# Optimization experiments

Hardware: AMD Instinct MI355X
Metric: run time of the kernel (lower is better)

## Reference

```python
import jax, jax.numpy as jnp
import numpy as np

OUT_H, OUT_W = 7, 7
SCALE = 0.25
S = 2  # sample_num per bin axis


def _bilinear(img, y, x):
    """Bilinearly sample img[..., H, W] at float coords (y, x).
    y, x have identical shape G; returns img.shape[:-2] + G.
    Matches RoIAlign CUDA interpolation (zero outside [-1, H]/[-1, W])."""
    H, W = img.shape[-2], img.shape[-1]
    valid = (y > -1.0) & (y < H) & (x > -1.0) & (x < W)
    y = jnp.clip(y, 0.0, H - 1)
    x = jnp.clip(x, 0.0, W - 1)
    y0 = jnp.floor(y).astype(jnp.int32)
    x0 = jnp.floor(x).astype(jnp.int32)
    y1 = jnp.minimum(y0 + 1, H - 1)
    x1 = jnp.minimum(x0 + 1, W - 1)
    ly = y - y0
    lx = x - x0
    hy, hx = 1.0 - ly, 1.0 - lx
    v = (hy * hx * img[..., y0, x0] + hy * lx * img[..., y0, x1]
         + ly * hx * img[..., y1, x0] + ly * lx * img[..., y1, x1])
    return jnp.where(valid, v, 0.0)


def setup_inputs() -> dict:
    key = jax.random.key(0)
    k1, k2, k3, k4, k5 = jax.random.split(key, 5)
    N, C, H, W = 2, 256, 200, 200
    R, MH, MW = 512, 128, 128
    features = jax.random.normal(k1, (N, C, H, W), jnp.float32)
    bidx = jax.random.randint(k2, (R,), 0, N)
    xy1 = jax.random.randint(k3, (R, 2), 0, 672)          # x1, y1 (image coords)
    wh = jax.random.randint(k4, (R, 2), 8, 128)           # box sizes in [8,128)
    xy2 = jnp.minimum(xy1 + wh - 1, 799)                  # x2, y2 inclusive
    rois = jnp.concatenate([bidx[:, None].astype(jnp.float32),
                            xy1.astype(jnp.float32),
                            xy2.astype(jnp.float32)], axis=1)  # [R,5]
    batch_masks = jax.random.uniform(k5, (R, MH, MW), jnp.float32)
    # zero-pad beyond each roi's (h, w), mimicking the list->dense packing
    hv = jnp.arange(MH)[None, :] < (xy2[:, 1] - xy1[:, 1] + 1)[:, None]
    wv = jnp.arange(MW)[None, :] < (xy2[:, 0] - xy1[:, 0] + 1)[:, None]
    batch_masks = batch_masks * (hv[:, :, None] & wv[:, None, :]).astype(jnp.float32)
    return {"features": features, "rois": rois, "batch_masks": batch_masks}


def reference(features, rois, batch_masks):
    """Mask-weighted RoIAlign: per-roi bilinear feature samples are weighted by
    the roi's shape mask (bilinearly sampled in roi-relative image coords),
    then average-pooled over the sub-sample grid of each output bin."""
    C = features.shape[1]

    def one_roi(roi, mask):
        b = roi[0].astype(jnp.int32)
        x1, y1, x2, y2 = roi[1], roi[2], roi[3], roi[4]
        roi_start_w = x1 * SCALE
        roi_start_h = y1 * SCALE
        roi_w = jnp.maximum((x2 - x1 + 1.0) * SCALE, 1.0)
        roi_h = jnp.maximum((y2 - y1 + 1.0) * SCALE, 1.0)
        bin_w = roi_w / OUT_W
        bin_h = roi_h / OUT_H
        # sub-sample offsets: (bin + (i+0.5)/S) for i in [0,S)  -> [OUT*S]
        offs = (jnp.arange(S, dtype=jnp.float32) + 0.5) / S
        ys = roi_start_h + (jnp.arange(OUT_H, dtype=jnp.float32)[:, None] + offs[None, :]).reshape(-1) * bin_h
        xs = roi_start_w + (jnp.arange(OUT_W, dtype=jnp.float32)[:, None] + offs[None, :]).reshape(-1) * bin_w
        yy, xx = jnp.meshgrid(ys, xs, indexing='ij')       # [OUT_H*S, OUT_W*S]
        feat = features[b]                                  # [C, H, W]
        vals = _bilinear(feat, yy, xx)                      # [C, OUT_H*S, OUT_W*S]
        # mask weight at the same sample point, in roi-relative image coords
        my = jnp.clip(yy / SCALE - y1, 0.0, y2 - y1)
        mx = jnp.clip(xx / SCALE - x1, 0.0, x2 - x1)
        wgt = _bilinear(mask, my, mx)                       # [OUT_H*S, OUT_W*S]
        v = (vals * wgt).reshape(C, OUT_H, S, OUT_W, S)
        return v.mean(axis=(2, 4))                          # [C, OUT_H, OUT_W]

    return jax.vmap(one_roi)(rois, batch_masks)             # [R, C, OUT_H, OUT_W]
```

## Files before the change

### kernel.cpp

```cpp
#include <hip/hip_runtime.h>


constexpr int   OUT_H = 7, OUT_W = 7;
constexpr int   NBIN  = OUT_H * OUT_W;
constexpr float SCALE = 0.25f;
constexpr int   S     = 2;
constexpr int   NSAMP = NBIN * S * S;
constexpr int   CG    = 8;
constexpr int   RDIM  = 34;
constexpr int   RCOLS = 40;
constexpr int   CST   = RDIM * RCOLS + 4;

typedef unsigned short ushort_t;

__device__ __forceinline__ ushort_t f2bf(float f) {
    unsigned u = __float_as_uint(f);
    u += 0x7fffu + ((u >> 16) & 1u);
    return (ushort_t)(u >> 16);
}
__device__ __forceinline__ float bf2f(ushort_t h) {
    return __uint_as_float(((unsigned)h) << 16);
}

__global__ __launch_bounds__(256, 6)
void roialign_direct_kernel(const float* __restrict__ features,
                            const float* __restrict__ rois,
                            const float* __restrict__ masks,
                            float*       __restrict__ out,
                            int C, int H, int W, int MH, int MW) {
    __shared__ __align__(16) ushort_t s_reg[CG * CST];
    __shared__ ushort4 s_idx[NSAMP];
    __shared__ float4  s_w[NSAMP];

    const int r   = blockIdx.x;
    const int cg  = blockIdx.y;
    const int tid = threadIdx.x;

    const float* roi = rois + (size_t)r * 5;
    const int   b  = (int)roi[0];
    const float x1 = roi[1], y1 = roi[2], x2 = roi[3], y2 = roi[4];

    const float roi_start_w = x1 * SCALE;
    const float roi_start_h = y1 * SCALE;
    const float roi_w = fmaxf((x2 - x1 + 1.0f) * SCALE, 1.0f);
    const float roi_h = fmaxf((y2 - y1 + 1.0f) * SCALE, 1.0f);
    const float bin_w = roi_w * (1.0f / OUT_W);
    const float bin_h = roi_h * (1.0f / OUT_H);

    int y_lo = (int)floorf(roi_start_h); y_lo = max(0, min(y_lo, H - 1));
    int x_lo = (int)floorf(roi_start_w); x_lo = max(0, min(x_lo, W - 1));
    const int y_hi = max(y_lo, min((int)floorf(roi_start_h + roi_h) + 1, H - 1));
    const int x_hi = max(x_lo, min((int)floorf(roi_start_w + roi_w) + 1, W - 1));
    const int rows  = min(y_hi - y_lo + 1, RDIM);
    const int x_lo4 = x_lo & ~3;
    const int cols4 = min((x_hi - x_lo4 + 4) >> 2, RCOLS / 4);

    {
        const int c8   = tid >> 5;
        const int lane = tid & 31;
        const float* src = features + ((size_t)b * C + (size_t)(cg * CG + c8)) * (size_t)(H * W);
        ushort_t* dst = s_reg + c8 * CST;
        const int items = rows * cols4;
        for (int it = lane; it < items; it += 32) {
            const int ry = it / cols4;
            const int k  = it - ry * cols4;
            const float4 v = *(const float4*)(src + (size_t)(y_lo + ry) * W + x_lo4 + 4 * k);
            ushort4 h;
            h.x = f2bf(v.x); h.y = f2bf(v.y); h.z = f2bf(v.z); h.w = f2bf(v.w);
            *(ushort4*)(dst + ry * RCOLS + 4 * k) = h;
        }
    }

    if (tid < NSAMP) {
        const int bin = tid >> 2;
        const int sub = tid & 3;
        const int ph  = bin / OUT_W, pw = bin % OUT_W;
        const int iy  = sub >> 1,   ix = sub & 1;

        const float yy = roi_start_h + ((float)ph + ((float)iy + 0.5f) * (1.0f / S)) * bin_h;
        const float xx = roi_start_w + ((float)pw + ((float)ix + 0.5f) * (1.0f / S)) * bin_w;

        const bool valid = (yy > -1.0f) && (yy < (float)H) && (xx > -1.0f) && (xx < (float)W);

        const float* msk = masks + (size_t)r * MH * MW;
        float my = fminf(fmaxf(yy * (1.0f / SCALE) - y1, 0.0f), y2 - y1);
        float mx = fminf(fmaxf(xx * (1.0f / SCALE) - x1, 0.0f), x2 - x1);
        my = fminf(fmaxf(my, 0.0f), (float)(MH - 1));
        mx = fminf(fmaxf(mx, 0.0f), (float)(MW - 1));
        const int my0 = (int)floorf(my), mx0 = (int)floorf(mx);
        const int my1 = min(my0 + 1, MH - 1), mx1 = min(mx0 + 1, MW - 1);
        const float mly = my - (float)my0, mlx = mx - (float)mx0;
        const float mhy = 1.0f - mly,      mhx = 1.0f - mlx;
        const float wgt = mhy * mhx * msk[my0 * MW + mx0] + mhy * mlx * msk[my0 * MW + mx1]
                        + mly * mhx * msk[my1 * MW + mx0] + mly * mlx * msk[my1 * MW + mx1];

        const float yc = fminf(fmaxf(yy, 0.0f), (float)(H - 1));
        const float xc = fminf(fmaxf(xx, 0.0f), (float)(W - 1));
        const int y0  = (int)floorf(yc), x0 = (int)floorf(xc);
        const int y1i = min(y0 + 1, H - 1), x1i = min(x0 + 1, W - 1);
        const float ly = yc - (float)y0, lx = xc - (float)x0;
        const float hy = 1.0f - ly,      hx = 1.0f - lx;

        const int ly0 = min(max(y0  - y_lo,  0), RDIM  - 1);
        const int ly1 = min(max(y1i - y_lo,  0), RDIM  - 1);
        const int lx0 = min(max(x0  - x_lo4, 0), RCOLS - 1);
        const int lx1 = min(max(x1i - x_lo4, 0), RCOLS - 1);

        const float scale_all = (valid ? wgt : 0.0f) * (1.0f / (float)(S * S));
        ushort4 ix4;
        ix4.x = (ushort_t)(ly0 * RCOLS + lx0);
        ix4.y = (ushort_t)(ly0 * RCOLS + lx1);
        ix4.z = (ushort_t)(ly1 * RCOLS + lx0);
        ix4.w = (ushort_t)(ly1 * RCOLS + lx1);
        s_idx[tid] = ix4;
        float4 w4;
        w4.x = hy * hx * scale_all;
        w4.y = hy * lx * scale_all;
        w4.z = ly * hx * scale_all;
        w4.w = ly * lx * scale_all;
        s_w[tid] = w4;
    }
    __syncthreads();

    const int c  = tid & 7;
    const int sg = tid >> 3;
    const ushort_t* creg = s_reg + c * CST;

    float acc0 = 0.0f, acc1 = 0.0f;
#pragma unroll
    for (int sub = 0; sub < 4; ++sub) {
        const int s = sg * 4 + sub;
        const ushort4 ix = s_idx[s];
        const float4  w  = s_w[s];
        acc0 += w.x * bf2f(creg[ix.x]) + w.y * bf2f(creg[ix.y])
              + w.z * bf2f(creg[ix.z]) + w.w * bf2f(creg[ix.w]);
    }
    const int bin1 = sg + 32;
    if (bin1 < NBIN) {
#pragma unroll
        for (int sub = 0; sub < 4; ++sub) {
            const int s = bin1 * 4 + sub;
            const ushort4 ix = s_idx[s];
            const float4  w  = s_w[s];
            acc1 += w.x * bf2f(creg[ix.x]) + w.y * bf2f(creg[ix.y])
                  + w.z * bf2f(creg[ix.z]) + w.w * bf2f(creg[ix.w]);
        }
    }
    __syncthreads();

    float* s_out = (float*)s_reg;
    s_out[c * NBIN + sg] = acc0;
    if (bin1 < NBIN) s_out[c * NBIN + bin1] = acc1;
    __syncthreads();

    float* outr = out + ((size_t)r * C + (size_t)cg * CG) * NBIN;
    for (int i = tid; i < CG * NBIN; i += 256)
        outr[i] = s_out[i];
}

__global__ __launch_bounds__(256)
void mask_roialign_kernel(const float* __restrict__ features,
                          const float* __restrict__ rois,
                          const float* __restrict__ masks,
                          float*       __restrict__ out,
                          int C, int H, int W, int MH, int MW) {
    int blk = blockIdx.x;
    int pw  = blk % OUT_W;
    int ph  = (blk / OUT_W) % OUT_H;
    int r   = blk / (OUT_W * OUT_H);
    int c   = threadIdx.x;
    if (c >= C) return;

    const float* roi = rois + (size_t)r * 5;
    int   b  = (int)roi[0];
    float x1 = roi[1], y1 = roi[2], x2 = roi[3], y2 = roi[4];

    float roi_start_w = x1 * SCALE;
    float roi_start_h = y1 * SCALE;
    float roi_w = fmaxf((x2 - x1 + 1.0f) * SCALE, 1.0f);
    float roi_h = fmaxf((y2 - y1 + 1.0f) * SCALE, 1.0f);
    float bin_w = roi_w / (float)OUT_W;
    float bin_h = roi_h / (float)OUT_H;

    const float* fch = features + ((size_t)b * C + c) * (size_t)(H * W);
    const float* msk = masks + (size_t)r * MH * MW;

    float acc = 0.0f;
#pragma unroll
    for (int iy = 0; iy < S; ++iy) {
        float yy = roi_start_h + ((float)ph + ((float)iy + 0.5f) / (float)S) * bin_h;
#pragma unroll
        for (int ix = 0; ix < S; ++ix) {
            float xx = roi_start_w + ((float)pw + ((float)ix + 0.5f) / (float)S) * bin_w;
            bool valid = (yy > -1.0f) && (yy < (float)H) && (xx > -1.0f) && (xx < (float)W);
            float my = fminf(fmaxf(yy / SCALE - y1, 0.0f), fminf(y2 - y1, (float)(MH - 1)));
            float mx = fminf(fmaxf(xx / SCALE - x1, 0.0f), fminf(x2 - x1, (float)(MW - 1)));
            int my0 = (int)floorf(my), mx0 = (int)floorf(mx);
            int my1 = min(my0 + 1, MH - 1), mx1 = min(mx0 + 1, MW - 1);
            float mly = my - my0, mlx = mx - mx0, mhy = 1.0f - mly, mhx = 1.0f - mlx;
            float wgt = mhy * mhx * msk[my0 * MW + mx0] + mhy * mlx * msk[my0 * MW + mx1]
                      + mly * mhx * msk[my1 * MW + mx0] + mly * mlx * msk[my1 * MW + mx1];
            if (valid) {
                float yc = fminf(fmaxf(yy, 0.0f), (float)(H - 1));
                float xc = fminf(fmaxf(xx, 0.0f), (float)(W - 1));
                int y0 = (int)floorf(yc), x0 = (int)floorf(xc);
                int y1i = min(y0 + 1, H - 1), x1i = min(x0 + 1, W - 1);
                float ly = yc - y0, lx = xc - x0, hy = 1.0f - ly, hx = 1.0f - lx;
                float v = hy * hx * fch[y0  * W + x0 ] + hy * lx * fch[y0  * W + x1i]
                        + ly * hx * fch[y1i * W + x0 ] + ly * lx * fch[y1i * W + x1i];
                acc += wgt * v;
            }
        }
    }
    out[((size_t)r * C + c) * (size_t)NBIN + ph * OUT_W + pw] = acc * (1.0f / (S * S));
}

extern "C" void kernel_launch(void* const* d_in, const int* in_sizes, int n_in,
                              void* d_out, int out_size, void* d_ws, size_t ws_size,
                              hipStream_t stream) {
    const float* features = (const float*)d_in[0];
    const float* rois     = (const float*)d_in[1];
    const float* masks    = (const float*)d_in[2];
    float*       out      = (float*)d_out;

    const int R  = in_sizes[1] / 5;
    const int C  = out_size / (R * NBIN);
    const int H  = 200, W = 200;
    const int MH = 128, MW = 128;

    (void)d_ws; (void)ws_size;

    if ((C % CG == 0) && (W % 4 == 0)) {
        roialign_direct_kernel<<<dim3(R, C / CG), dim3(256), 0, stream>>>(
            features, rois, masks, out, C, H, W, MH, MW);
    } else {
        mask_roialign_kernel<<<dim3(R * NBIN), dim3(256), 0, stream>>>(
            features, rois, masks, out, C, H, W, MH, MW);
    }
}
```

Baseline: 186.6 us.

## Interleave channel pairs as packed bf16 in LDS and gather both per load

The shared-memory tile now stores two channels interleaved per pixel as a packed 32-bit bf16 pair. Each compute thread handles one channel pair and one bin, so every 32-bit LDS gather yields two channel values and halves the number of gathers. The staging loop loads the even and odd channel rows together and replaces the integer divide with a float-reciprocal estimate plus a correction step. The compute phase now uses only 196 of 256 threads, and the index offsets are prescaled to byte offsets.

```diff
diff --git a/kernel.cpp b/kernel.cpp
--- a/kernel.cpp
+++ b/kernel.cpp
@@ -7,9 +7,11 @@
 constexpr int   S     = 2;
 constexpr int   NSAMP = NBIN * S * S;
 constexpr int   CG    = 8;
+constexpr int   NPAIR = CG / 2;
 constexpr int   RDIM  = 34;
 constexpr int   RCOLS = 40;
-constexpr int   CST   = RDIM * RCOLS + 4;
+constexpr int   NPIX  = RDIM * RCOLS;
+constexpr int   PSTRIDE = NPIX * 2 + 4;
 
 typedef unsigned short ushort_t;
 
@@ -17,9 +19,6 @@
     unsigned u = __float_as_uint(f);
     u += 0x7fffu + ((u >> 16) & 1u);
     return (ushort_t)(u >> 16);
-}
-__device__ __forceinline__ float bf2f(ushort_t h) {
-    return __uint_as_float(((unsigned)h) << 16);
 }
 
 __global__ __launch_bounds__(256, 6)
@@ -28,7 +27,7 @@
                             const float* __restrict__ masks,
                             float*       __restrict__ out,
                             int C, int H, int W, int MH, int MW) {
-    __shared__ __align__(16) ushort_t s_reg[CG * CST];
+    __shared__ __align__(16) ushort_t s_reg[NPAIR * PSTRIDE];
     __shared__ ushort4 s_idx[NSAMP];
     __shared__ float4  s_w[NSAMP];
 
@@ -56,18 +55,32 @@
     const int cols4 = min((x_hi - x_lo4 + 4) >> 2, RCOLS / 4);
 
     {
-        const int c8   = tid >> 5;
+        const int g    = tid >> 5;
         const int lane = tid & 31;
-        const float* src = features + ((size_t)b * C + (size_t)(cg * CG + c8)) * (size_t)(H * W);
-        ushort_t* dst = s_reg + c8 * CST;
+        const int pr   = g >> 1;
+        const int part = g & 1;
+        const size_t HWs = (size_t)H * W;
+        const float* srcE = features + ((size_t)b * C + (size_t)(cg * CG + 2 * pr)) * HWs
+                          + (size_t)y_lo * W + x_lo4;
+        const float* srcO = srcE + HWs;
+        unsigned* dp32base = (unsigned*)(s_reg + pr * PSTRIDE);
         const int items = rows * cols4;
-        for (int it = lane; it < items; it += 32) {
-            const int ry = it / cols4;
-            const int k  = it - ry * cols4;
-            const float4 v = *(const float4*)(src + (size_t)(y_lo + ry) * W + x_lo4 + 4 * k);
-            ushort4 h;
-            h.x = f2bf(v.x); h.y = f2bf(v.y); h.z = f2bf(v.z); h.w = f2bf(v.w);
-            *(ushort4*)(dst + ry * RCOLS + 4 * k) = h;
+        const float rcp = 1.0f / (float)cols4;
+        for (int it = lane + part * 32; it < items; it += 64) {
+            int ry = (int)((float)it * rcp);
+            int k  = it - ry * cols4;
+            if (k >= cols4) { ry++; k -= cols4; }
+            if (k < 0)      { ry--; k += cols4; }
+            const float4 vE = *(const float4*)(srcE + ry * W + 4 * k);
+            const float4 vO = *(const float4*)(srcO + ry * W + 4 * k);
+            const int pix = ry * RCOLS + 4 * k;
+            uint2 a, c2;
+            a.x  = (unsigned)f2bf(vE.x) | ((unsigned)f2bf(vO.x) << 16);
+            a.y  = (unsigned)f2bf(vE.y) | ((unsigned)f2bf(vO.y) << 16);
+            c2.x = (unsigned)f2bf(vE.z) | ((unsigned)f2bf(vO.z) << 16);
+            c2.y = (unsigned)f2bf(vE.w) | ((unsigned)f2bf(vO.w) << 16);
+            *(uint2*)(dp32base + pix)     = a;
+            *(uint2*)(dp32base + pix + 2) = c2;
         }
     }
 
@@ -108,10 +121,10 @@
 
         const float scale_all = (valid ? wgt : 0.0f) * (1.0f / (float)(S * S));
         ushort4 ix4;
-        ix4.x = (ushort_t)(ly0 * RCOLS + lx0);
-        ix4.y = (ushort_t)(ly0 * RCOLS + lx1);
-        ix4.z = (ushort_t)(ly1 * RCOLS + lx0);
-        ix4.w = (ushort_t)(ly1 * RCOLS + lx1);
+        ix4.x = (ushort_t)((ly0 * RCOLS + lx0) * 4);
+        ix4.y = (ushort_t)((ly0 * RCOLS + lx1) * 4);
+        ix4.z = (ushort_t)((ly1 * RCOLS + lx0) * 4);
+        ix4.w = (ushort_t)((ly1 * RCOLS + lx1) * 4);
         s_idx[tid] = ix4;
         float4 w4;
         w4.x = hy * hx * scale_all;
@@ -122,35 +135,37 @@
     }
     __syncthreads();
 
-    const int c  = tid & 7;
-    const int sg = tid >> 3;
-    const ushort_t* creg = s_reg + c * CST;
-
-    float acc0 = 0.0f, acc1 = 0.0f;
-#pragma unroll
-    for (int sub = 0; sub < 4; ++sub) {
-        const int s = sg * 4 + sub;
-        const ushort4 ix = s_idx[s];
-        const float4  w  = s_w[s];
-        acc0 += w.x * bf2f(creg[ix.x]) + w.y * bf2f(creg[ix.y])
-              + w.z * bf2f(creg[ix.z]) + w.w * bf2f(creg[ix.w]);
-    }
-    const int bin1 = sg + 32;
-    if (bin1 < NBIN) {
+    float accE = 0.0f, accO = 0.0f;
+    const int pr  = tid & 3;
+    const int bin = tid >> 2;
+    if (tid < NSAMP) {
+        const char* base = (const char*)s_reg + pr * (PSTRIDE * 2);
 #pragma unroll
         for (int sub = 0; sub < 4; ++sub) {
-            const int s = bin1 * 4 + sub;
-            const ushort4 ix = s_idx[s];
-            const float4  w  = s_w[s];
-            acc1 += w.x * bf2f(creg[ix.x]) + w.y * bf2f(creg[ix.y])
-                  + w.z * bf2f(creg[ix.z]) + w.w * bf2f(creg[ix.w]);
+            const int s = bin * 4 + sub;
+            const ushort4 off = s_idx[s];
+            const float4  w   = s_w[s];
+            const unsigned q0 = *(const unsigned*)(base + off.x);
+            const unsigned q1 = *(const unsigned*)(base + off.y);
+            const unsigned q2 = *(const unsigned*)(base + off.z);
+            const unsigned q3 = *(const unsigned*)(base + off.w);
+            accE = fmaf(w.x, __uint_as_float(q0 << 16),          accE);
+            accO = fmaf(w.x, __uint_as_float(q0 & 0xffff0000u),  accO);
+            accE = fmaf(w.y, __uint_as_float(q1 << 16),          accE);
+            accO = fmaf(w.y, __uint_as_float(q1 & 0xffff0000u),  accO);
+            accE = fmaf(w.z, __uint_as_float(q2 << 16),          accE);
+            accO = fmaf(w.z, __uint_as_float(q2 & 0xffff0000u),  accO);
+            accE = fmaf(w.w, __uint_as_float(q3 << 16),          accE);
+            accO = fmaf(w.w, __uint_as_float(q3 & 0xffff0000u),  accO);
         }
     }
     __syncthreads();
 
     float* s_out = (float*)s_reg;
-    s_out[c * NBIN + sg] = acc0;
-    if (bin1 < NBIN) s_out[c * NBIN + bin1] = acc1;
+    if (tid < NSAMP) {
+        s_out[(2 * pr + 0) * NBIN + bin] = accE;
+        s_out[(2 * pr + 1) * NBIN + bin] = accO;
+    }
     __syncthreads();
 
     float* outr = out + ((size_t)r * C + (size_t)cg * CG) * NBIN;
```

New measurement: 179.1 us. 4.0% less time.

## Stage fp32 feature tiles via direct global-to-LDS loads and reorder grid

Applied to the files above, without the earlier changes.

Replaces the register-staged bf16 conversion of the feature tile with asynchronous global_load_lds transfers that write fp32 rows straight into shared memory, using a compact per-roi row stride. Mask loads are issued before the feature copy so their latency overlaps it, and sample offsets are now byte offsets into the fp32 tile. The grid is transposed so the channel-group blocks of the same roi are adjacent, which may improve locality, and the occupancy hint is lowered to fit the doubled LDS footprint. This removes the bf16 rounding and its conversion cost, but it doubles shared memory per block and reduces how many blocks can be resident.

```diff
diff --git a/kernel.cpp b/kernel.cpp
--- a/kernel.cpp
+++ b/kernel.cpp
@@ -8,32 +8,24 @@
 constexpr int   NSAMP = NBIN * S * S;
 constexpr int   CG    = 8;
 constexpr int   RDIM  = 34;
-constexpr int   RCOLS = 40;
-constexpr int   CST   = RDIM * RCOLS + 4;
+constexpr int   RCOLS4 = 10;
+constexpr int   MAXIT  = RDIM * RCOLS4;
+constexpr int   CH_DW  = MAXIT * 4 + 4;
 
 typedef unsigned short ushort_t;
 
-__device__ __forceinline__ ushort_t f2bf(float f) {
-    unsigned u = __float_as_uint(f);
-    u += 0x7fffu + ((u >> 16) & 1u);
-    return (ushort_t)(u >> 16);
-}
-__device__ __forceinline__ float bf2f(ushort_t h) {
-    return __uint_as_float(((unsigned)h) << 16);
-}
-
-__global__ __launch_bounds__(256, 6)
+__global__ __launch_bounds__(256, 3)
 void roialign_direct_kernel(const float* __restrict__ features,
                             const float* __restrict__ rois,
                             const float* __restrict__ masks,
                             float*       __restrict__ out,
                             int C, int H, int W, int MH, int MW) {
-    __shared__ __align__(16) ushort_t s_reg[CG * CST];
+    __shared__ __align__(16) float s_reg[CG * CH_DW];
     __shared__ ushort4 s_idx[NSAMP];
     __shared__ float4  s_w[NSAMP];
 
-    const int r   = blockIdx.x;
-    const int cg  = blockIdx.y;
+    const int cgp = blockIdx.x;
+    const int r   = blockIdx.y;
     const int tid = threadIdx.x;
 
     const float* roi = rois + (size_t)r * 5;
@@ -53,34 +45,18 @@
     const int x_hi = max(x_lo, min((int)floorf(roi_start_w + roi_w) + 1, W - 1));
     const int rows  = min(y_hi - y_lo + 1, RDIM);
     const int x_lo4 = x_lo & ~3;
-    const int cols4 = min((x_hi - x_lo4 + 4) >> 2, RCOLS / 4);
-
-    {
-        const int c8   = tid >> 5;
-        const int lane = tid & 31;
-        const float* src = features + ((size_t)b * C + (size_t)(cg * CG + c8)) * (size_t)(H * W);
-        ushort_t* dst = s_reg + c8 * CST;
-        const int items = rows * cols4;
-        for (int it = lane; it < items; it += 32) {
-            const int ry = it / cols4;
-            const int k  = it - ry * cols4;
-            const float4 v = *(const float4*)(src + (size_t)(y_lo + ry) * W + x_lo4 + 4 * k);
-            ushort4 h;
-            h.x = f2bf(v.x); h.y = f2bf(v.y); h.z = f2bf(v.z); h.w = f2bf(v.w);
-            *(ushort4*)(dst + ry * RCOLS + 4 * k) = h;
-        }
-    }
-
+    const int cols4 = min((x_hi - x_lo4 + 4) >> 2, RCOLS4);
+    const int rs_dw = cols4 << 2;
+
+    float yy = 0.f, xx = 0.f, m00 = 0.f, m01 = 0.f, m10 = 0.f, m11 = 0.f;
+    float mly = 0.f, mlx = 0.f;
     if (tid < NSAMP) {
         const int bin = tid >> 2;
         const int sub = tid & 3;
         const int ph  = bin / OUT_W, pw = bin % OUT_W;
         const int iy  = sub >> 1,   ix = sub & 1;
-
-        const float yy = roi_start_h + ((float)ph + ((float)iy + 0.5f) * (1.0f / S)) * bin_h;
-        const float xx = roi_start_w + ((float)pw + ((float)ix + 0.5f) * (1.0f / S)) * bin_w;
-
-        const bool valid = (yy > -1.0f) && (yy < (float)H) && (xx > -1.0f) && (xx < (float)W);
+        yy = roi_start_h + ((float)ph + ((float)iy + 0.5f) * (1.0f / S)) * bin_h;
+        xx = roi_start_w + ((float)pw + ((float)ix + 0.5f) * (1.0f / S)) * bin_w;
 
         const float* msk = masks + (size_t)r * MH * MW;
         float my = fminf(fmaxf(yy * (1.0f / SCALE) - y1, 0.0f), y2 - y1);
@@ -89,10 +65,49 @@
         mx = fminf(fmaxf(mx, 0.0f), (float)(MW - 1));
         const int my0 = (int)floorf(my), mx0 = (int)floorf(mx);
         const int my1 = min(my0 + 1, MH - 1), mx1 = min(mx0 + 1, MW - 1);
-        const float mly = my - (float)my0, mlx = mx - (float)mx0;
-        const float mhy = 1.0f - mly,      mhx = 1.0f - mlx;
-        const float wgt = mhy * mhx * msk[my0 * MW + mx0] + mhy * mlx * msk[my0 * MW + mx1]
-                        + mly * mhx * msk[my1 * MW + mx0] + mly * mlx * msk[my1 * MW + mx1];
+        mly = my - (float)my0; mlx = mx - (float)mx0;
+        m00 = msk[my0 * MW + mx0];
+        m01 = msk[my0 * MW + mx1];
+        m10 = msk[my1 * MW + mx0];
+        m11 = msk[my1 * MW + mx1];
+    }
+
+    {
+        const int wv   = tid >> 6;
+        const int lane = tid & 63;
+        const int items = rows * cols4;
+        const int nch   = (items + 63) >> 6;
+        const int imax  = max(items - 64, 0);
+        const float rcp = 1.0f / (float)cols4;
+        const size_t HWs = (size_t)H * W;
+#pragma unroll
+        for (int cc = 0; cc < 2; ++cc) {
+            const int ch = 2 * wv + cc;
+            const float* src0 = features
+                + ((size_t)b * C + (size_t)(cgp * CG + ch)) * HWs
+                + (size_t)y_lo * W + x_lo4;
+            float* lbase = s_reg + ch * CH_DW;
+            for (int j = 0; j < nch; ++j) {
+                const int bi = min(j << 6, imax);
+                const int it = min(bi + lane, items - 1);
+                int ry = (int)((float)it * rcp);
+                int k  = it - ry * cols4;
+                if (k < 0)           { --ry; k += cols4; }
+                else if (k >= cols4) { ++ry; k -= cols4; }
+                const float* src = src0 + (ry * W + (k << 2));
+                __builtin_amdgcn_global_load_lds(
+                    (const __attribute__((address_space(1))) unsigned int*)src,
+                    (__attribute__((address_space(3))) unsigned int*)(lbase + (bi << 2)),
+                    16, 0, 0);
+            }
+        }
+    }
+
+    if (tid < NSAMP) {
+        const bool valid = (yy > -1.0f) && (yy < (float)H) && (xx > -1.0f) && (xx < (float)W);
+        const float mhy = 1.0f - mly, mhx = 1.0f - mlx;
+        const float wgt = mhy * mhx * m00 + mhy * mlx * m01
+                        + mly * mhx * m10 + mly * mlx * m11;
 
         const float yc = fminf(fmaxf(yy, 0.0f), (float)(H - 1));
         const float xc = fminf(fmaxf(xx, 0.0f), (float)(W - 1));
@@ -101,18 +116,18 @@
         const float ly = yc - (float)y0, lx = xc - (float)x0;
         const float hy = 1.0f - ly,      hx = 1.0f - lx;
 
-        const int ly0 = min(max(y0  - y_lo,  0), RDIM  - 1);
-        const int ly1 = min(max(y1i - y_lo,  0), RDIM  - 1);
-        const int lx0 = min(max(x0  - x_lo4, 0), RCOLS - 1);
-        const int lx1 = min(max(x1i - x_lo4, 0), RCOLS - 1);
+        const int ly0 = min(max(y0  - y_lo,  0), rows - 1);
+        const int ly1 = min(max(y1i - y_lo,  0), rows - 1);
+        const int lx0 = min(max(x0  - x_lo4, 0), rs_dw - 1);
+        const int lx1 = min(max(x1i - x_lo4, 0), rs_dw - 1);
 
         const float scale_all = (valid ? wgt : 0.0f) * (1.0f / (float)(S * S));
-        ushort4 ix4;
-        ix4.x = (ushort_t)(ly0 * RCOLS + lx0);
-        ix4.y = (ushort_t)(ly0 * RCOLS + lx1);
-        ix4.z = (ushort_t)(ly1 * RCOLS + lx0);
-        ix4.w = (ushort_t)(ly1 * RCOLS + lx1);
-        s_idx[tid] = ix4;
+        ushort4 o;
+        o.x = (ushort_t)((ly0 * rs_dw + lx0) << 2);
+        o.y = (ushort_t)((ly0 * rs_dw + lx1) << 2);
+        o.z = (ushort_t)((ly1 * rs_dw + lx0) << 2);
+        o.w = (ushort_t)((ly1 * rs_dw + lx1) << 2);
+        s_idx[tid] = o;
         float4 w4;
         w4.x = hy * hx * scale_all;
         w4.y = hy * lx * scale_all;
@@ -124,26 +139,30 @@
 
     const int c  = tid & 7;
     const int sg = tid >> 3;
-    const ushort_t* creg = s_reg + c * CST;
+    const char* creg = (const char*)(s_reg + c * CH_DW);
 
     float acc0 = 0.0f, acc1 = 0.0f;
 #pragma unroll
     for (int sub = 0; sub < 4; ++sub) {
-        const int s = sg * 4 + sub;
-        const ushort4 ix = s_idx[s];
-        const float4  w  = s_w[s];
-        acc0 += w.x * bf2f(creg[ix.x]) + w.y * bf2f(creg[ix.y])
-              + w.z * bf2f(creg[ix.z]) + w.w * bf2f(creg[ix.w]);
+        const int s0 = (sg << 2) + sub;
+        const ushort4 o = s_idx[s0];
+        const float4  w = s_w[s0];
+        acc0 = fmaf(w.x, *(const float*)(creg + o.x), acc0);
+        acc0 = fmaf(w.y, *(const float*)(creg + o.y), acc0);
+        acc0 = fmaf(w.z, *(const float*)(creg + o.z), acc0);
+        acc0 = fmaf(w.w, *(const float*)(creg + o.w), acc0);
     }
     const int bin1 = sg + 32;
     if (bin1 < NBIN) {
 #pragma unroll
         for (int sub = 0; sub < 4; ++sub) {
-            const int s = bin1 * 4 + sub;
-            const ushort4 ix = s_idx[s];
-            const float4  w  = s_w[s];
-            acc1 += w.x * bf2f(creg[ix.x]) + w.y * bf2f(creg[ix.y])
-                  + w.z * bf2f(creg[ix.z]) + w.w * bf2f(creg[ix.w]);
+            const int s1 = (bin1 << 2) + sub;
+            const ushort4 o = s_idx[s1];
+            const float4  w = s_w[s1];
+            acc1 = fmaf(w.x, *(const float*)(creg + o.x), acc1);
+            acc1 = fmaf(w.y, *(const float*)(creg + o.y), acc1);
+            acc1 = fmaf(w.z, *(const float*)(creg + o.z), acc1);
+            acc1 = fmaf(w.w, *(const float*)(creg + o.w), acc1);
         }
     }
     __syncthreads();
@@ -153,7 +172,7 @@
     if (bin1 < NBIN) s_out[c * NBIN + bin1] = acc1;
     __syncthreads();
 
-    float* outr = out + ((size_t)r * C + (size_t)cg * CG) * NBIN;
+    float* outr = out + ((size_t)r * C + (size_t)cgp * CG) * NBIN;
     for (int i = tid; i < CG * NBIN; i += 256)
         outr[i] = s_out[i];
 }
@@ -231,7 +250,7 @@
     (void)d_ws; (void)ws_size;
 
     if ((C % CG == 0) && (W % 4 == 0)) {
-        roialign_direct_kernel<<<dim3(R, C / CG), dim3(256), 0, stream>>>(
+        roialign_direct_kernel<<<dim3(C / CG, R), dim3(256), 0, stream>>>(
             features, rois, masks, out, C, H, W, MH, MW);
     } else {
         mask_roialign_kernel<<<dim3(R * NBIN), dim3(256), 0, stream>>>(
```

Result: slower. 197.3 us (+5.7%).
